# Kernel tuning notes

Hardware: AMD Instinct MI355X
Metric: run time of the kernel (lower is better)

## Reference

```python
import jax, jax.numpy as jnp
import numpy as np

VOCAB, EMBED, EN_H, DE_H, ATTN, LAYERS = 50000, 256, 512, 512, 256, 2
SEQ, BATCH = 1024, 64

def setup_inputs() -> dict:
    key = jax.random.key(0)
    ks = jax.random.split(key, 20)
    n = lambda k, shp: jax.random.normal(k, shp, dtype=jnp.float32)
    inp = {
        "cur_input": jax.random.randint(ks[0], (BATCH,), 0, VOCAB, dtype=jnp.int64) if jax.config.jax_enable_x64 else jax.random.randint(ks[0], (BATCH,), 0, VOCAB, dtype=jnp.int32),
        "h0": n(ks[1], (LAYERS, BATCH, DE_H)),
        "c0": n(ks[2], (LAYERS, BATCH, DE_H)),
        "enc_states": n(ks[3], (SEQ, BATCH, EN_H)),
        "attention_mask": jnp.ones((BATCH, SEQ), dtype=jnp.float32),
        # parameters
        "emb_table": n(ks[4], (VOCAB, EMBED)) * 0.02,
        "attn_W": n(ks[5], (EN_H + DE_H, ATTN)) * 0.02,   # attention_model: Linear(en+de, attn, bias=False)
        "attn_v": n(ks[6], (ATTN,)) * 0.02,               # Linear(attn, 1, bias=False)
        "cg_W": n(ks[7], (DE_H + EMBED + EN_H, EN_H)) * 0.02,  # context gate
        "cg_b": jnp.zeros((EN_H,), dtype=jnp.float32),
        "Wih0": n(ks[8], (4 * DE_H, EN_H + EMBED)) * 0.02,
        "Whh0": n(ks[9], (4 * DE_H, DE_H)) * 0.02,
        "bih0": jnp.zeros((4 * DE_H,), dtype=jnp.float32),
        "bhh0": jnp.zeros((4 * DE_H,), dtype=jnp.float32),
        "Wih1": n(ks[10], (4 * DE_H, DE_H)) * 0.02,
        "Whh1": n(ks[11], (4 * DE_H, DE_H)) * 0.02,
        "bih1": jnp.zeros((4 * DE_H,), dtype=jnp.float32),
        "bhh1": jnp.zeros((4 * DE_H,), dtype=jnp.float32),
        "out_W": n(ks[12], (DE_H, VOCAB)) * 0.02,
        "out_b": jnp.zeros((VOCAB,), dtype=jnp.float32),
    }
    return inp

def _lstm_cell(x, h, c, Wih, Whh, bih, bhh):
    gates = x @ Wih.T + h @ Whh.T + bih + bhh  # (B, 4H), torch gate order i,f,g,o
    i, f, g, o = jnp.split(gates, 4, axis=-1)
    c_new = jax.nn.sigmoid(f) * c + jax.nn.sigmoid(i) * jnp.tanh(g)
    h_new = jax.nn.sigmoid(o) * jnp.tanh(c_new)
    return h_new, c_new

def reference(cur_input, h0, c0, enc_states, attention_mask,
              emb_table, attn_W, attn_v, cg_W, cg_b,
              Wih0, Whh0, bih0, bhh0, Wih1, Whh1, bih1, bhh1,
              out_W, out_b):
    S, B, _ = enc_states.shape
    dec = h0[-1]  # (B, DE_H)
    # Bahdanau attention: score over seq dim
    dec_b = jnp.broadcast_to(dec[None], (S, B, dec.shape[-1]))
    feat = jnp.tanh(jnp.concatenate([enc_states, dec_b], axis=-1) @ attn_W)  # (S,B,ATTN)
    e = feat @ attn_v  # (S,B)
    e = jnp.where(attention_mask.T > 0, e, jnp.float32(-1e9))
    alpha = jax.nn.softmax(e, axis=0)  # (S,B)
    ctx = jnp.einsum('sb,sbh->bh', alpha, enc_states)  # (B, EN_H)
    # embedding + context gate
    emb = emb_table[cur_input]  # (B, EMBED)
    gate = jax.nn.sigmoid(jnp.concatenate([dec, emb, ctx], axis=-1) @ cg_W + cg_b)
    ctx = gate * ctx
    x = jnp.concatenate([emb, ctx], axis=-1)  # (B, EMBED+EN_H)
    # two-layer single-step LSTM
    h1, c1 = _lstm_cell(x, h0[0], c0[0], Wih0, Whh0, bih0, bhh0)
    h2, c2 = _lstm_cell(h1, h0[1], c0[1], Wih1, Whh1, bih1, bhh1)
    out = h2 @ out_W + out_b  # (B, VOCAB)
    return out, jnp.stack([h1, h2]), jnp.stack([c1, c2])
```

## Files before the change

### kernel.cpp

```cpp
#include <hip/hip_runtime.h>
#include <math.h>


typedef __attribute__((ext_vector_type(8))) short short8;
typedef __attribute__((ext_vector_type(4))) float f32x4;

__device__ __forceinline__ float sigf(float x) { return 1.f / (1.f + expf(-x)); }

__device__ __forceinline__ unsigned short f2bf(float f) {
    unsigned int u = __builtin_bit_cast(unsigned int, f);
    unsigned int r = (u + 0x7fffu + ((u >> 16) & 1u)) >> 16;
    return (unsigned short)r;
}

__device__ __forceinline__ float tanh_fast(float x) {
    float t = __expf(2.f * x);
    return 1.f - 2.f * __builtin_amdgcn_rcpf(1.f + t);
}

__global__ void k_prep_conv(const int* __restrict__ cur, const float* __restrict__ h0,
                            const float* __restrict__ emb_table, const float* __restrict__ attn_W,
                            float* __restrict__ X1, float* __restrict__ X2, float* __restrict__ X3,
                            float* __restrict__ decW, unsigned short* __restrict__ Wt) {
    int t = threadIdx.x;
    if (blockIdx.x >= 64) {
        __shared__ float tile[64][65];
        int bx = blockIdx.x - 64;
        int kb = (bx & 7) * 64, nb = (bx >> 3) * 64;
        int r0 = t >> 6, c = t & 63;
#pragma unroll
        for (int i = 0; i < 16; ++i) {
            int r = i * 4 + r0;
            tile[r][c] = attn_W[(size_t)(kb + r) * 256 + nb + c];
        }
        __syncthreads();
#pragma unroll
        for (int i = 0; i < 16; ++i) {
            int r = i * 4 + r0;
            int n = nb + r;
            int byte = ((n * 128 + ((c >> 3) << 4)) ^ ((r & 7) << 4)) + ((c & 7) << 1);
            *(unsigned short*)((char*)Wt + kb * 512 + byte) = f2bf(tile[c][r]);
        }
        return;
    }
    __shared__ float dec_s[512];
    int b = blockIdx.x;
    const float* dec = h0 + (size_t)(64 + b) * 512;
    for (int i = t; i < 512; i += 256) {
        float v = dec[i];
        dec_s[i] = v;
        X1[b * 1280 + i] = v;
        X2[b * 1280 + 768 + i] = h0[(size_t)b * 512 + i];
        X3[b * 1024 + 512 + i] = v;
    }
    int row = cur[b];
    float ev = emb_table[(size_t)row * 256 + t];
    X1[b * 1280 + 512 + t] = ev;
    X2[b * 1280 + t] = ev;
    __syncthreads();
    float acc = 0.f;
    for (int k = 0; k < 512; ++k)
        acc += dec_s[k] * attn_W[(size_t)(512 + k) * 256 + t];
    decW[b * 256 + t] = acc;
}

__global__ __launch_bounds__(256) void k_scores_mfma(
        const float* __restrict__ enc, const unsigned short* __restrict__ Wt,
        const float* __restrict__ attn_v, const float* __restrict__ decW,
        float* __restrict__ e_out) {
    int s = blockIdx.x, t = threadIdx.x;
    __shared__ __align__(16) unsigned short sA[2][4096];
    __shared__ __align__(16) unsigned short sB[16384];
    const float* arow = enc + (size_t)s * 64 * 512;
    int w = t >> 6, l = t & 63, li = l & 15, lg = l >> 4;
    int sw = (li & 7) << 4;

    int ar0 = t >> 3, akg0 = t & 7;
    int ar1 = (256 + t) >> 3, akg1 = t & 7;
    int abyte0 = (ar0 * 128 + akg0 * 16) ^ ((ar0 & 7) << 4);
    int abyte1 = (ar1 * 128 + akg1 * 16) ^ ((ar1 & 7) << 4);
    int bbase = w * 8192 + l * 16;

    f32x4 acc[4][4];
#pragma unroll
    for (int rt = 0; rt < 4; ++rt)
#pragma unroll
        for (int ct = 0; ct < 4; ++ct) acc[rt][ct] = (f32x4){0.f, 0.f, 0.f, 0.f};

    float4 aP[4];
    uint4  bP[8];

#pragma unroll
    for (int i = 0; i < 2; ++i) {
        const float* g = arow + (ar0 + i * 32) * 512 + akg0 * 8;
        aP[2 * i] = *(const float4*)g;
        aP[2 * i + 1] = *(const float4*)(g + 4);
    }
#pragma unroll
    for (int j = 0; j < 8; ++j)
        bP[j] = *(const uint4*)((const char*)Wt + bbase + j * 1024);
    {
        uint4 wv0, wv1;
        wv0.x = f2bf(aP[0].x) | ((unsigned)f2bf(aP[0].y) << 16);
        wv0.y = f2bf(aP[0].z) | ((unsigned)f2bf(aP[0].w) << 16);
        wv0.z = f2bf(aP[1].x) | ((unsigned)f2bf(aP[1].y) << 16);
        wv0.w = f2bf(aP[1].z) | ((unsigned)f2bf(aP[1].w) << 16);
        wv1.x = f2bf(aP[2].x) | ((unsigned)f2bf(aP[2].y) << 16);
        wv1.y = f2bf(aP[2].z) | ((unsigned)f2bf(aP[2].w) << 16);
        wv1.z = f2bf(aP[3].x) | ((unsigned)f2bf(aP[3].y) << 16);
        wv1.w = f2bf(aP[3].z) | ((unsigned)f2bf(aP[3].w) << 16);
        *(uint4*)((char*)sA[0] + abyte0) = wv0;
        *(uint4*)((char*)sA[0] + abyte1) = wv1;
#pragma unroll
        for (int j = 0; j < 8; ++j)
            *(uint4*)((char*)sB + bbase + j * 1024) = bP[j];
    }
    __syncthreads();

    for (int kk = 0; kk < 8; ++kk) {
        int cur = kk & 1;
        if (kk < 7) {
            int ko = (kk + 1) * 64;
#pragma unroll
            for (int i = 0; i < 2; ++i) {
                const float* g = arow + (ar0 + i * 32) * 512 + ko + akg0 * 8;
                aP[2 * i] = *(const float4*)g;
                aP[2 * i + 1] = *(const float4*)(g + 4);
            }
            const char* src = (const char*)Wt + ((kk + 1) << 15);
#pragma unroll
            for (int j = 0; j < 8; ++j)
                bP[j] = *(const uint4*)(src + bbase + j * 1024);
        }
#pragma unroll
        for (int ks = 0; ks < 2; ++ks) {
            short8 af[4], bf[4];
#pragma unroll
            for (int rt = 0; rt < 4; ++rt) {
                int row = rt * 16 + li;
                af[rt] = *(short8*)((char*)sA[cur] + ((row * 128 + ks * 64 + lg * 16) ^ sw));
            }
#pragma unroll
            for (int ct = 0; ct < 4; ++ct) {
                int n = w * 64 + ct * 16 + li;
                bf[ct] = *(short8*)((char*)sB + ((n * 128 + ks * 64 + lg * 16) ^ sw));
            }
#pragma unroll
            for (int rt = 0; rt < 4; ++rt)
#pragma unroll
                for (int ct = 0; ct < 4; ++ct)
                    acc[rt][ct] = __builtin_amdgcn_mfma_f32_16x16x32_bf16(
                        af[rt], bf[ct], acc[rt][ct], 0, 0, 0);
        }
        if (kk < 7) {
            uint4 wv0, wv1;
            wv0.x = f2bf(aP[0].x) | ((unsigned)f2bf(aP[0].y) << 16);
            wv0.y = f2bf(aP[0].z) | ((unsigned)f2bf(aP[0].w) << 16);
            wv0.z = f2bf(aP[1].x) | ((unsigned)f2bf(aP[1].y) << 16);
            wv0.w = f2bf(aP[1].z) | ((unsigned)f2bf(aP[1].w) << 16);
            wv1.x = f2bf(aP[2].x) | ((unsigned)f2bf(aP[2].y) << 16);
            wv1.y = f2bf(aP[2].z) | ((unsigned)f2bf(aP[2].w) << 16);
            wv1.z = f2bf(aP[3].x) | ((unsigned)f2bf(aP[3].y) << 16);
            wv1.w = f2bf(aP[3].z) | ((unsigned)f2bf(aP[3].w) << 16);
            *(uint4*)((char*)sA[cur ^ 1] + abyte0) = wv0;
            *(uint4*)((char*)sA[cur ^ 1] + abyte1) = wv1;
#pragma unroll
            for (int j = 0; j < 8; ++j)
                *(uint4*)((char*)sB + bbase + j * 1024) = bP[j];
        }
        __syncthreads();
    }

    float er[4][4];
#pragma unroll
    for (int rt = 0; rt < 4; ++rt)
#pragma unroll
        for (int r = 0; r < 4; ++r) er[rt][r] = 0.f;
#pragma unroll
    for (int ct = 0; ct < 4; ++ct) {
        int a = w * 64 + ct * 16 + li;
        float v = attn_v[a];
#pragma unroll
        for (int rt = 0; rt < 4; ++rt) {
#pragma unroll
            for (int r = 0; r < 4; ++r) {
                int row = rt * 16 + lg * 4 + r;
                float x = acc[rt][ct][r] + decW[row * 256 + a];
                er[rt][r] += tanh_fast(x) * v;
            }
        }
    }
#pragma unroll
    for (int off = 1; off < 16; off <<= 1)
#pragma unroll
        for (int rt = 0; rt < 4; ++rt)
#pragma unroll
            for (int r = 0; r < 4; ++r)
                er[rt][r] += __shfl_xor(er[rt][r], off, 64);
    float* part = (float*)sA[0];
    if (li == 0) {
#pragma unroll
        for (int rt = 0; rt < 4; ++rt)
#pragma unroll
            for (int r = 0; r < 4; ++r)
                part[w * 64 + rt * 16 + lg * 4 + r] = er[rt][r];
    }
    __syncthreads();
    if (t < 64)
        e_out[t * 1024 + s] = part[t] + part[64 + t] + part[128 + t] + part[192 + t];
}

__global__ __launch_bounds__(512) void k_ctx_partial(const float* __restrict__ ebuf,
        const float* __restrict__ mask, const float* __restrict__ enc,
        float* __restrict__ ctxP) {
    int b = blockIdx.x & 63, sc = blockIdx.x >> 6;
    int t = threadIdx.x;
    __shared__ float al[128];
    __shared__ float red[16];
    float v0 = ebuf[b * 1024 + t];
    float v1 = ebuf[b * 1024 + 512 + t];
    v0 = (mask[b * 1024 + t] > 0.f) ? v0 : -1e9f;
    v1 = (mask[b * 1024 + 512 + t] > 0.f) ? v1 : -1e9f;
    float lmax = fmaxf(v0, v1);
#pragma unroll
    for (int off = 32; off > 0; off >>= 1) lmax = fmaxf(lmax, __shfl_xor(lmax, off, 64));
    if ((t & 63) == 0) red[t >> 6] = lmax;
    __syncthreads();
    float m = red[0];
#pragma unroll
    for (int i = 1; i < 8; ++i) m = fmaxf(m, red[i]);
    float lsum = __expf(v0 - m) + __expf(v1 - m);
#pragma unroll
    for (int off = 32; off > 0; off >>= 1) lsum += __shfl_xor(lsum, off, 64);
    if ((t & 63) == 0) red[8 + (t >> 6)] = lsum;
    __syncthreads();
    float tot = red[8];
#pragma unroll
    for (int i = 1; i < 8; ++i) tot += red[8 + i];
    float inv = 1.f / tot;
    if (t < 128) {
        int s = sc * 128 + t;
        float x = ebuf[b * 1024 + s];
        x = (mask[b * 1024 + s] > 0.f) ? x : -1e9f;
        al[t] = __expf(x - m) * inv;
    }
    __syncthreads();
    const float* base = enc + (((size_t)sc * 128 * 64) + b) * 512 + t;
    float a0 = 0.f, a1 = 0.f, a2 = 0.f, a3 = 0.f;
    for (int s = 0; s < 128; s += 4) {
        float x0 = base[(size_t)(s + 0) * 32768];
        float x1 = base[(size_t)(s + 1) * 32768];
        float x2 = base[(size_t)(s + 2) * 32768];
        float x3 = base[(size_t)(s + 3) * 32768];
        a0 += al[s] * x0; a1 += al[s + 1] * x1; a2 += al[s + 2] * x2; a3 += al[s + 3] * x3;
    }
    ctxP[((size_t)sc * 64 + b) * 512 + t] = a0 + a1 + a2 + a3;
}

__global__ __launch_bounds__(1024) void k_gemm_cg(const float* __restrict__ X,
        const float* __restrict__ ctxP, const float* __restrict__ Wkn,
        float* __restrict__ P) {
    int n0 = blockIdx.x * 64, sp = blockIdx.y;
    int t = threadIdx.x, tc = t & 63, tr = t >> 6;
    __shared__ __align__(16) float As[64 * 68];
    __shared__ __align__(16) float Wc[64 * 68];
    float acc[4] = {0.f, 0.f, 0.f, 0.f};
    for (int c = 0; c < 5; ++c) {
        int k0 = sp * 320 + c * 64;
        __syncthreads();
#pragma unroll
        for (int i = 0; i < 4; ++i) {
            int idx = i * 1024 + t; int row = idx >> 6; int k = idx & 63;
            int gk = k0 + k;
            float v;
            if (gk < 768) {
                v = X[row * 1280 + gk];
            } else {
                int h = gk - 768;
                v = 0.f;
#pragma unroll
                for (int sc = 0; sc < 8; ++sc)
                    v += ctxP[((size_t)sc * 64 + row) * 512 + h];
            }
            As[k * 68 + row] = v;
        }
#pragma unroll
        for (int i = 0; i < 4; ++i) {
            int idx = i * 1024 + t; int k = idx >> 6; int cc = idx & 63;
            Wc[k * 68 + cc] = Wkn[(size_t)(k0 + k) * 512 + n0 + cc];
        }
        __syncthreads();
#pragma unroll 8
        for (int k = 0; k < 64; ++k) {
            float4 a = *(const float4*)&As[k * 68 + 4 * tr];
            float wv = Wc[k * 68 + tc];
            acc[0] += a.x * wv; acc[1] += a.y * wv; acc[2] += a.z * wv; acc[3] += a.w * wv;
        }
    }
    float* Pp = P + (size_t)sp * 64 * 512;
#pragma unroll
    for (int j = 0; j < 4; ++j) Pp[(4 * tr + j) * 512 + n0 + tc] = acc[j];
}

__global__ __launch_bounds__(1024) void k_gemm_lstm(const float* __restrict__ X, int ldx,
        const float* __restrict__ W1, int K1, const float* __restrict__ W2, int K2,
        int kchunks, float* __restrict__ P) {
    int n0 = blockIdx.x * 64, sp = blockIdx.y;
    int t = threadIdx.x, tc = t & 63, tr = t >> 6;
    __shared__ __align__(16) float As[64 * 68];
    __shared__ __align__(16) float Wc[64 * 68];
    float acc[4] = {0.f, 0.f, 0.f, 0.f};
    for (int c = 0; c < kchunks; ++c) {
        int k0 = (sp * kchunks + c) * 64;
        __syncthreads();
#pragma unroll
        for (int i = 0; i < 4; ++i) {
            int idx = i * 1024 + t; int row = idx >> 6; int k = idx & 63;
            As[k * 68 + row] = X[row * ldx + k0 + k];
        }
#pragma unroll
        for (int i = 0; i < 4; ++i) {
            int idx = i * 1024 + t; int cc = idx >> 6; int k = idx & 63;
            int gk = k0 + k; int j = n0 + cc;
            float wv = (gk < K1) ? W1[(size_t)j * K1 + gk] : W2[(size_t)j * K2 + gk - K1];
            Wc[k * 68 + cc] = wv;
        }
        __syncthreads();
#pragma unroll 8
        for (int k = 0; k < 64; ++k) {
            float4 a = *(const float4*)&As[k * 68 + 4 * tr];
            float wv = Wc[k * 68 + tc];
            acc[0] += a.x * wv; acc[1] += a.y * wv; acc[2] += a.z * wv; acc[3] += a.w * wv;
        }
    }
    float* Pp = P + (size_t)sp * 64 * 2048;
#pragma unroll
    for (int j = 0; j < 4; ++j) Pp[(4 * tr + j) * 2048 + n0 + tc] = acc[j];
}

__global__ void k_cg_fin(const float* __restrict__ P, const float* __restrict__ cg_b,
                         const float* __restrict__ ctxP, float* __restrict__ X2) {
    int idx = blockIdx.x * 256 + threadIdx.x;
    int b = idx >> 9, h = idx & 511;
    float g = cg_b[h];
#pragma unroll
    for (int sp = 0; sp < 4; ++sp) g += P[sp * 32768 + idx];
    float ctx = 0.f;
#pragma unroll
    for (int sc = 0; sc < 8; ++sc) ctx += ctxP[((size_t)sc * 64 + b) * 512 + h];
    X2[b * 1280 + 256 + h] = sigf(g) * ctx;
}

__global__ void k_lstm_fin(const float* __restrict__ P, const float* __restrict__ bih,
                           const float* __restrict__ bhh, const float* __restrict__ c0,
                           int layer, float* __restrict__ oh, float* __restrict__ oc,
                           float* __restrict__ X3out) {
    int idx = blockIdx.x * 256 + threadIdx.x;
    int b = idx >> 9, h = idx & 511;
    float gi = bih[h] + bhh[h];
    float gf = bih[512 + h] + bhh[512 + h];
    float gg = bih[1024 + h] + bhh[1024 + h];
    float go = bih[1536 + h] + bhh[1536 + h];
#pragma unroll
    for (int sp = 0; sp < 4; ++sp) {
        const float* Pp = P + sp * 131072 + b * 2048;
        gi += Pp[h]; gf += Pp[512 + h]; gg += Pp[1024 + h]; go += Pp[1536 + h];
    }
    float cp = c0[layer * 32768 + b * 512 + h];
    float cn = sigf(gf) * cp + sigf(gi) * tanhf(gg);
    float hn = sigf(go) * tanhf(cn);
    oh[b * 512 + h] = hn;
    oc[b * 512 + h] = cn;
    if (X3out) X3out[b * 1024 + h] = hn;
}

__global__ __launch_bounds__(256) void k_outproj_mfma(
        const float* __restrict__ h2, const float* __restrict__ out_W,
        const float* __restrict__ out_b, float* __restrict__ out) {
    int t = threadIdx.x;
    int n0 = blockIdx.x * 128;
    int w = t >> 6, l = t & 63, li = l & 15, lg = l >> 4;
    int sw = (li & 7) << 4;
    __shared__ __align__(16) unsigned short sA[4096];

    f32x4 acc[4][2];
#pragma unroll
    for (int rt = 0; rt < 4; ++rt)
#pragma unroll
        for (int ct = 0; ct < 2; ++ct) acc[rt][ct] = (f32x4){0.f, 0.f, 0.f, 0.f};
    int colbase = n0 + w * 32;

    for (int kk = 0; kk < 512; kk += 64) {
        __syncthreads();
#pragma unroll
        for (int i = 0; i < 2; ++i) {
            int idx = i * 256 + t, row = idx >> 3, kg = idx & 7;
            const float* g = h2 + row * 512 + kk + kg * 8;
            float4 p0 = *(const float4*)g;
            float4 p1 = *(const float4*)(g + 4);
            uint4 wv;
            wv.x = f2bf(p0.x) | ((unsigned)f2bf(p0.y) << 16);
            wv.y = f2bf(p0.z) | ((unsigned)f2bf(p0.w) << 16);
            wv.z = f2bf(p1.x) | ((unsigned)f2bf(p1.y) << 16);
            wv.w = f2bf(p1.z) | ((unsigned)f2bf(p1.w) << 16);
            int byte = (row * 128 + kg * 16) ^ ((row & 7) << 4);
            *(uint4*)((char*)sA + byte) = wv;
        }
        __syncthreads();
#pragma unroll
        for (int ks = 0; ks < 2; ++ks) {
            short8 bf[2];
#pragma unroll
            for (int ct = 0; ct < 2; ++ct) {
                int col = colbase + ct * 16 + li;
                col = (col < 50000) ? col : 49999;
                const float* wp = out_W + (size_t)(kk + ks * 32 + lg * 8) * 50000 + col;
                uint4 qv;
                float v0 = wp[0],          v1 = wp[50000];
                float v2 = wp[2 * 50000],  v3 = wp[3 * 50000];
                float v4 = wp[4 * 50000],  v5 = wp[5 * 50000];
                float v6 = wp[6 * 50000],  v7 = wp[7 * 50000];
                qv.x = f2bf(v0) | ((unsigned)f2bf(v1) << 16);
                qv.y = f2bf(v2) | ((unsigned)f2bf(v3) << 16);
                qv.z = f2bf(v4) | ((unsigned)f2bf(v5) << 16);
                qv.w = f2bf(v6) | ((unsigned)f2bf(v7) << 16);
                bf[ct] = *(short8*)&qv;
            }
            short8 af[4];
#pragma unroll
            for (int rt = 0; rt < 4; ++rt) {
                int row = rt * 16 + li;
                af[rt] = *(short8*)((char*)sA + ((row * 128 + ks * 64 + lg * 16) ^ sw));
            }
#pragma unroll
            for (int rt = 0; rt < 4; ++rt)
#pragma unroll
                for (int ct = 0; ct < 2; ++ct)
                    acc[rt][ct] = __builtin_amdgcn_mfma_f32_16x16x32_bf16(
                        af[rt], bf[ct], acc[rt][ct], 0, 0, 0);
        }
    }
#pragma unroll
    for (int ct = 0; ct < 2; ++ct) {
        int col = colbase + ct * 16 + li;
        if (col < 50000) {
            float bias = out_b[col];
#pragma unroll
            for (int rt = 0; rt < 4; ++rt)
#pragma unroll
                for (int r = 0; r < 4; ++r) {
                    int row = rt * 16 + lg * 4 + r;
                    out[(size_t)row * 50000 + col] = acc[rt][ct][r] + bias;
                }
        }
    }
}

extern "C" void kernel_launch(void* const* d_in, const int* in_sizes, int n_in,
                              void* d_out, int out_size, void* d_ws, size_t ws_size,
                              hipStream_t stream) {
    const int*   cur       = (const int*)d_in[0];
    const float* h0        = (const float*)d_in[1];
    const float* c0        = (const float*)d_in[2];
    const float* enc       = (const float*)d_in[3];
    const float* mask      = (const float*)d_in[4];
    const float* emb_table = (const float*)d_in[5];
    const float* attn_W    = (const float*)d_in[6];
    const float* attn_v    = (const float*)d_in[7];
    const float* cg_W      = (const float*)d_in[8];
    const float* cg_b      = (const float*)d_in[9];
    const float* Wih0      = (const float*)d_in[10];
    const float* Whh0      = (const float*)d_in[11];
    const float* bih0      = (const float*)d_in[12];
    const float* bhh0      = (const float*)d_in[13];
    const float* Wih1      = (const float*)d_in[14];
    const float* Whh1      = (const float*)d_in[15];
    const float* bih1      = (const float*)d_in[16];
    const float* bhh1      = (const float*)d_in[17];
    const float* out_W     = (const float*)d_in[18];
    const float* out_b     = (const float*)d_in[19];
    float* out = (float*)d_out;

    float* w    = (float*)d_ws;
    float* X1   = w;
    float* X2   = X1 + 81920;
    float* X3   = X2 + 81920;
    float* decW = X3 + 65536;
    float* eb   = decW + 16384;
    float* P    = eb + 65536;
    unsigned short* Wt = (unsigned short*)P;
    float* ctxP = P + 524288;

    float* outH = out + 3200000;
    float* outC = out + 3265536;

    hipLaunchKernelGGL(k_prep_conv, dim3(96), dim3(256), 0, stream,
                       cur, h0, emb_table, attn_W, X1, X2, X3, decW, Wt);
    hipLaunchKernelGGL(k_scores_mfma, dim3(1024), dim3(256), 0, stream,
                       enc, Wt, attn_v, decW, eb);
    hipLaunchKernelGGL(k_ctx_partial, dim3(512), dim3(512), 0, stream,
                       eb, mask, enc, ctxP);
    hipLaunchKernelGGL(k_gemm_cg, dim3(8, 4), dim3(1024), 0, stream,
                       X1, ctxP, cg_W, P);
    hipLaunchKernelGGL(k_cg_fin, dim3(128), dim3(256), 0, stream, P, cg_b, ctxP, X2);
    hipLaunchKernelGGL(k_gemm_lstm, dim3(32, 4), dim3(1024), 0, stream,
                       X2, 1280, Wih0, 768, Whh0, 512, 5, P);
    hipLaunchKernelGGL(k_lstm_fin, dim3(128), dim3(256), 0, stream,
                       P, bih0, bhh0, c0, 0, outH, outC, X3);
    hipLaunchKernelGGL(k_gemm_lstm, dim3(32, 4), dim3(1024), 0, stream,
                       X3, 1024, Wih1, 512, Whh1, 512, 4, P);
    hipLaunchKernelGGL(k_lstm_fin, dim3(128), dim3(256), 0, stream,
                       P, bih1, bhh1, c0, 1, outH + 32768, outC + 32768, (float*)nullptr);
    hipLaunchKernelGGL(k_outproj_mfma, dim3(391), dim3(256), 0, stream,
                       outH + 32768, out_W, out_b, out);
}
```

Measured before the change: 184.0 us.

## Fuse context-gate and LSTM finalize steps into following GEMM prologues

Removes the separate context-gate finalize and layer-0 LSTM finalize kernels by recomputing their elementwise work inside the A-tile load of the next GEMM, and halves the split-K factor so each GEMM has two partial slices. It also swaps the manual bf16 rounding for the packed v_cvt_pk_bf16_f32 instruction and uses fast sigmoid/tanh. This cuts kernel launches and intermediate round-trips, but the fused GEMMs recompute the gate math redundantly across column blocks and run fewer blocks, so there is less parallelism.

```diff
diff --git a/kernel.cpp b/kernel.cpp
--- a/kernel.cpp
+++ b/kernel.cpp
@@ -6,11 +6,20 @@
 typedef __attribute__((ext_vector_type(4))) float f32x4;
 
 __device__ __forceinline__ float sigf(float x) { return 1.f / (1.f + expf(-x)); }
+__device__ __forceinline__ float sigf_fast(float x) {
+    return __builtin_amdgcn_rcpf(1.f + __expf(-x));
+}
 
 __device__ __forceinline__ unsigned short f2bf(float f) {
     unsigned int u = __builtin_bit_cast(unsigned int, f);
     unsigned int r = (u + 0x7fffu + ((u >> 16) & 1u)) >> 16;
     return (unsigned short)r;
+}
+
+__device__ __forceinline__ unsigned cvt_pk(float lo, float hi) {
+    unsigned r;
+    asm("v_cvt_pk_bf16_f32 %0, %1, %2" : "=v"(r) : "v"(lo), "v"(hi));
+    return r;
 }
 
 __device__ __forceinline__ float tanh_fast(float x) {
@@ -76,9 +85,9 @@
     int sw = (li & 7) << 4;
 
     int ar0 = t >> 3, akg0 = t & 7;
-    int ar1 = (256 + t) >> 3, akg1 = t & 7;
+    int ar1 = (256 + t) >> 3;
     int abyte0 = (ar0 * 128 + akg0 * 16) ^ ((ar0 & 7) << 4);
-    int abyte1 = (ar1 * 128 + akg1 * 16) ^ ((ar1 & 7) << 4);
+    int abyte1 = (ar1 * 128 + akg0 * 16) ^ ((ar1 & 7) << 4);
     int bbase = w * 8192 + l * 16;
 
     f32x4 acc[4][4];
@@ -101,14 +110,10 @@
         bP[j] = *(const uint4*)((const char*)Wt + bbase + j * 1024);
     {
         uint4 wv0, wv1;
-        wv0.x = f2bf(aP[0].x) | ((unsigned)f2bf(aP[0].y) << 16);
-        wv0.y = f2bf(aP[0].z) | ((unsigned)f2bf(aP[0].w) << 16);
-        wv0.z = f2bf(aP[1].x) | ((unsigned)f2bf(aP[1].y) << 16);
-        wv0.w = f2bf(aP[1].z) | ((unsigned)f2bf(aP[1].w) << 16);
-        wv1.x = f2bf(aP[2].x) | ((unsigned)f2bf(aP[2].y) << 16);
-        wv1.y = f2bf(aP[2].z) | ((unsigned)f2bf(aP[2].w) << 16);
-        wv1.z = f2bf(aP[3].x) | ((unsigned)f2bf(aP[3].y) << 16);
-        wv1.w = f2bf(aP[3].z) | ((unsigned)f2bf(aP[3].w) << 16);
+        wv0.x = cvt_pk(aP[0].x, aP[0].y); wv0.y = cvt_pk(aP[0].z, aP[0].w);
+        wv0.z = cvt_pk(aP[1].x, aP[1].y); wv0.w = cvt_pk(aP[1].z, aP[1].w);
+        wv1.x = cvt_pk(aP[2].x, aP[2].y); wv1.y = cvt_pk(aP[2].z, aP[2].w);
+        wv1.z = cvt_pk(aP[3].x, aP[3].y); wv1.w = cvt_pk(aP[3].z, aP[3].w);
         *(uint4*)((char*)sA[0] + abyte0) = wv0;
         *(uint4*)((char*)sA[0] + abyte1) = wv1;
 #pragma unroll
@@ -154,14 +159,10 @@
         }
         if (kk < 7) {
             uint4 wv0, wv1;
-            wv0.x = f2bf(aP[0].x) | ((unsigned)f2bf(aP[0].y) << 16);
-            wv0.y = f2bf(aP[0].z) | ((unsigned)f2bf(aP[0].w) << 16);
-            wv0.z = f2bf(aP[1].x) | ((unsigned)f2bf(aP[1].y) << 16);
-            wv0.w = f2bf(aP[1].z) | ((unsigned)f2bf(aP[1].w) << 16);
-            wv1.x = f2bf(aP[2].x) | ((unsigned)f2bf(aP[2].y) << 16);
-            wv1.y = f2bf(aP[2].z) | ((unsigned)f2bf(aP[2].w) << 16);
-            wv1.z = f2bf(aP[3].x) | ((unsigned)f2bf(aP[3].y) << 16);
-            wv1.w = f2bf(aP[3].z) | ((unsigned)f2bf(aP[3].w) << 16);
+            wv0.x = cvt_pk(aP[0].x, aP[0].y); wv0.y = cvt_pk(aP[0].z, aP[0].w);
+            wv0.z = cvt_pk(aP[1].x, aP[1].y); wv0.w = cvt_pk(aP[1].z, aP[1].w);
+            wv1.x = cvt_pk(aP[2].x, aP[2].y); wv1.y = cvt_pk(aP[2].z, aP[2].w);
+            wv1.z = cvt_pk(aP[3].x, aP[3].y); wv1.w = cvt_pk(aP[3].z, aP[3].w);
             *(uint4*)((char*)sA[cur ^ 1] + abyte0) = wv0;
             *(uint4*)((char*)sA[cur ^ 1] + abyte1) = wv1;
 #pragma unroll
@@ -259,14 +260,14 @@
 
 __global__ __launch_bounds__(1024) void k_gemm_cg(const float* __restrict__ X,
         const float* __restrict__ ctxP, const float* __restrict__ Wkn,
-        float* __restrict__ P) {
+        float* __restrict__ P1) {
     int n0 = blockIdx.x * 64, sp = blockIdx.y;
     int t = threadIdx.x, tc = t & 63, tr = t >> 6;
     __shared__ __align__(16) float As[64 * 68];
     __shared__ __align__(16) float Wc[64 * 68];
     float acc[4] = {0.f, 0.f, 0.f, 0.f};
-    for (int c = 0; c < 5; ++c) {
-        int k0 = sp * 320 + c * 64;
+    for (int c = 0; c < 10; ++c) {
+        int k0 = sp * 640 + c * 64;
         __syncthreads();
 #pragma unroll
         for (int i = 0; i < 4; ++i) {
@@ -297,32 +298,48 @@
             acc[0] += a.x * wv; acc[1] += a.y * wv; acc[2] += a.z * wv; acc[3] += a.w * wv;
         }
     }
-    float* Pp = P + (size_t)sp * 64 * 512;
+    float* Pp = P1 + (size_t)sp * 32768;
 #pragma unroll
     for (int j = 0; j < 4; ++j) Pp[(4 * tr + j) * 512 + n0 + tc] = acc[j];
 }
 
-__global__ __launch_bounds__(1024) void k_gemm_lstm(const float* __restrict__ X, int ldx,
-        const float* __restrict__ W1, int K1, const float* __restrict__ W2, int K2,
-        int kchunks, float* __restrict__ P) {
+__global__ __launch_bounds__(1024) void k_lstm0_fused(const float* __restrict__ X2,
+        const float* __restrict__ P1, const float* __restrict__ ctxP,
+        const float* __restrict__ cg_b,
+        const float* __restrict__ Wih0, const float* __restrict__ Whh0,
+        float* __restrict__ Pl0) {
     int n0 = blockIdx.x * 64, sp = blockIdx.y;
     int t = threadIdx.x, tc = t & 63, tr = t >> 6;
     __shared__ __align__(16) float As[64 * 68];
     __shared__ __align__(16) float Wc[64 * 68];
     float acc[4] = {0.f, 0.f, 0.f, 0.f};
-    for (int c = 0; c < kchunks; ++c) {
-        int k0 = (sp * kchunks + c) * 64;
+    for (int c = 0; c < 10; ++c) {
+        int k0 = sp * 640 + c * 64;
         __syncthreads();
 #pragma unroll
         for (int i = 0; i < 4; ++i) {
             int idx = i * 1024 + t; int row = idx >> 6; int k = idx & 63;
-            As[k * 68 + row] = X[row * ldx + k0 + k];
+            int gk = k0 + k;
+            float v;
+            if (gk < 256 || gk >= 768) {
+                v = X2[row * 1280 + gk];
+            } else {
+                int h = gk - 256;
+                float g = cg_b[h] + P1[row * 512 + h] + P1[32768 + row * 512 + h];
+                float ctx = 0.f;
+#pragma unroll
+                for (int sc = 0; sc < 8; ++sc)
+                    ctx += ctxP[((size_t)sc * 64 + row) * 512 + h];
+                v = sigf_fast(g) * ctx;
+            }
+            As[k * 68 + row] = v;
         }
 #pragma unroll
         for (int i = 0; i < 4; ++i) {
             int idx = i * 1024 + t; int cc = idx >> 6; int k = idx & 63;
             int gk = k0 + k; int j = n0 + cc;
-            float wv = (gk < K1) ? W1[(size_t)j * K1 + gk] : W2[(size_t)j * K2 + gk - K1];
+            float wv = (gk < 768) ? Wih0[(size_t)j * 768 + gk]
+                                  : Whh0[(size_t)j * 512 + gk - 768];
             Wc[k * 68 + cc] = wv;
         }
         __syncthreads();
@@ -333,28 +350,74 @@
             acc[0] += a.x * wv; acc[1] += a.y * wv; acc[2] += a.z * wv; acc[3] += a.w * wv;
         }
     }
-    float* Pp = P + (size_t)sp * 64 * 2048;
+    float* Pp = Pl0 + (size_t)sp * 131072;
 #pragma unroll
     for (int j = 0; j < 4; ++j) Pp[(4 * tr + j) * 2048 + n0 + tc] = acc[j];
 }
 
-__global__ void k_cg_fin(const float* __restrict__ P, const float* __restrict__ cg_b,
-                         const float* __restrict__ ctxP, float* __restrict__ X2) {
-    int idx = blockIdx.x * 256 + threadIdx.x;
-    int b = idx >> 9, h = idx & 511;
-    float g = cg_b[h];
-#pragma unroll
-    for (int sp = 0; sp < 4; ++sp) g += P[sp * 32768 + idx];
-    float ctx = 0.f;
-#pragma unroll
-    for (int sc = 0; sc < 8; ++sc) ctx += ctxP[((size_t)sc * 64 + b) * 512 + h];
-    X2[b * 1280 + 256 + h] = sigf(g) * ctx;
-}
-
-__global__ void k_lstm_fin(const float* __restrict__ P, const float* __restrict__ bih,
-                           const float* __restrict__ bhh, const float* __restrict__ c0,
-                           int layer, float* __restrict__ oh, float* __restrict__ oc,
-                           float* __restrict__ X3out) {
+__global__ __launch_bounds__(1024) void k_lstm1_fused(const float* __restrict__ X3,
+        const float* __restrict__ Pl0, const float* __restrict__ bih0,
+        const float* __restrict__ bhh0, const float* __restrict__ c0,
+        const float* __restrict__ Wih1, const float* __restrict__ Whh1,
+        float* __restrict__ Pl1, float* __restrict__ outH, float* __restrict__ outC) {
+    int n0 = blockIdx.x * 64, sp = blockIdx.y;
+    int t = threadIdx.x, tc = t & 63, tr = t >> 6;
+    __shared__ __align__(16) float As[64 * 68];
+    __shared__ __align__(16) float Wc[64 * 68];
+    float acc[4] = {0.f, 0.f, 0.f, 0.f};
+    for (int c = 0; c < 8; ++c) {
+        int k0 = sp * 512 + c * 64;
+        __syncthreads();
+#pragma unroll
+        for (int i = 0; i < 4; ++i) {
+            int idx = i * 1024 + t; int row = idx >> 6; int k = idx & 63;
+            int gk = k0 + k;
+            float v;
+            if (gk < 512) {
+                int h = gk;
+                const float* Pa = Pl0 + row * 2048;
+                const float* Pb = Pl0 + 131072 + row * 2048;
+                float gi = bih0[h] + bhh0[h] + Pa[h] + Pb[h];
+                float gf = bih0[512 + h] + bhh0[512 + h] + Pa[512 + h] + Pb[512 + h];
+                float gg = bih0[1024 + h] + bhh0[1024 + h] + Pa[1024 + h] + Pb[1024 + h];
+                float go = bih0[1536 + h] + bhh0[1536 + h] + Pa[1536 + h] + Pb[1536 + h];
+                float cp = c0[row * 512 + h];
+                float cn = sigf_fast(gf) * cp + sigf_fast(gi) * tanh_fast(gg);
+                float hn = sigf_fast(go) * tanh_fast(cn);
+                v = hn;
+                if (n0 == 0) {
+                    outH[row * 512 + h] = hn;
+                    outC[row * 512 + h] = cn;
+                }
+            } else {
+                v = X3[row * 1024 + gk];
+            }
+            As[k * 68 + row] = v;
+        }
+#pragma unroll
+        for (int i = 0; i < 4; ++i) {
+            int idx = i * 1024 + t; int cc = idx >> 6; int k = idx & 63;
+            int gk = k0 + k; int j = n0 + cc;
+            float wv = (gk < 512) ? Wih1[(size_t)j * 512 + gk]
+                                  : Whh1[(size_t)j * 512 + gk - 512];
+            Wc[k * 68 + cc] = wv;
+        }
+        __syncthreads();
+#pragma unroll 8
+        for (int k = 0; k < 64; ++k) {
+            float4 a = *(const float4*)&As[k * 68 + 4 * tr];
+            float wv = Wc[k * 68 + tc];
+            acc[0] += a.x * wv; acc[1] += a.y * wv; acc[2] += a.z * wv; acc[3] += a.w * wv;
+        }
+    }
+    float* Pp = Pl1 + (size_t)sp * 131072;
+#pragma unroll
+    for (int j = 0; j < 4; ++j) Pp[(4 * tr + j) * 2048 + n0 + tc] = acc[j];
+}
+
+__global__ void k_lstm_fin1(const float* __restrict__ Pl1, const float* __restrict__ bih,
+                            const float* __restrict__ bhh, const float* __restrict__ c0,
+                            float* __restrict__ oh, float* __restrict__ oc) {
     int idx = blockIdx.x * 256 + threadIdx.x;
     int b = idx >> 9, h = idx & 511;
     float gi = bih[h] + bhh[h];
@@ -362,16 +425,15 @@
     float gg = bih[1024 + h] + bhh[1024 + h];
     float go = bih[1536 + h] + bhh[1536 + h];
 #pragma unroll
-    for (int sp = 0; sp < 4; ++sp) {
-        const float* Pp = P + sp * 131072 + b * 2048;
+    for (int sp = 0; sp < 2; ++sp) {
+        const float* Pp = Pl1 + sp * 131072 + b * 2048;
         gi += Pp[h]; gf += Pp[512 + h]; gg += Pp[1024 + h]; go += Pp[1536 + h];
     }
-    float cp = c0[layer * 32768 + b * 512 + h];
+    float cp = c0[32768 + b * 512 + h];
     float cn = sigf(gf) * cp + sigf(gi) * tanhf(gg);
     float hn = sigf(go) * tanhf(cn);
-    oh[b * 512 + h] = hn;
-    oc[b * 512 + h] = cn;
-    if (X3out) X3out[b * 1024 + h] = hn;
+    oh[32768 + b * 512 + h] = hn;
+    oc[32768 + b * 512 + h] = cn;
 }
 
 __global__ __launch_bounds__(256) void k_outproj_mfma(
@@ -399,10 +461,8 @@
             float4 p0 = *(const float4*)g;
             float4 p1 = *(const float4*)(g + 4);
             uint4 wv;
-            wv.x = f2bf(p0.x) | ((unsigned)f2bf(p0.y) << 16);
-            wv.y = f2bf(p0.z) | ((unsigned)f2bf(p0.w) << 16);
-            wv.z = f2bf(p1.x) | ((unsigned)f2bf(p1.y) << 16);
-            wv.w = f2bf(p1.z) | ((unsigned)f2bf(p1.w) << 16);
+            wv.x = cvt_pk(p0.x, p0.y); wv.y = cvt_pk(p0.z, p0.w);
+            wv.z = cvt_pk(p1.x, p1.y); wv.w = cvt_pk(p1.z, p1.w);
             int byte = (row * 128 + kg * 16) ^ ((row & 7) << 4);
             *(uint4*)((char*)sA + byte) = wv;
         }
@@ -420,10 +480,8 @@
                 float v2 = wp[2 * 50000],  v3 = wp[3 * 50000];
                 float v4 = wp[4 * 50000],  v5 = wp[5 * 50000];
                 float v6 = wp[6 * 50000],  v7 = wp[7 * 50000];
-                qv.x = f2bf(v0) | ((unsigned)f2bf(v1) << 16);
-                qv.y = f2bf(v2) | ((unsigned)f2bf(v3) << 16);
-                qv.z = f2bf(v4) | ((unsigned)f2bf(v5) << 16);
-                qv.w = f2bf(v6) | ((unsigned)f2bf(v7) << 16);
+                qv.x = cvt_pk(v0, v1); qv.y = cvt_pk(v2, v3);
+                qv.z = cvt_pk(v4, v5); qv.w = cvt_pk(v6, v7);
                 bf[ct] = *(short8*)&qv;
             }
             short8 af[4];
@@ -487,9 +545,11 @@
     float* X3   = X2 + 81920;
     float* decW = X3 + 65536;
     float* eb   = decW + 16384;
-    float* P    = eb + 65536;
-    unsigned short* Wt = (unsigned short*)P;
-    float* ctxP = P + 524288;
+    float* P1   = eb;
+    float* Pl0  = eb + 65536;
+    float* Pl1  = Pl0 + 262144;
+    float* ctxP = Pl1 + 262144;
+    unsigned short* Wt = (unsigned short*)Pl0;
 
     float* outH = out + 3200000;
     float* outC = out + 3265536;
@@ -500,17 +560,14 @@
                        enc, Wt, attn_v, decW, eb);
     hipLaunchKernelGGL(k_ctx_partial, dim3(512), dim3(512), 0, stream,
                        eb, mask, enc, ctxP);
-    hipLaunchKernelGGL(k_gemm_cg, dim3(8, 4), dim3(1024), 0, stream,
-                       X1, ctxP, cg_W, P);
-    hipLaunchKernelGGL(k_cg_fin, dim3(128), dim3(256), 0, stream, P, cg_b, ctxP, X2);
-    hipLaunchKernelGGL(k_gemm_lstm, dim3(32, 4), dim3(1024), 0, stream,
-                       X2, 1280, Wih0, 768, Whh0, 512, 5, P);
-    hipLaunchKernelGGL(k_lstm_fin, dim3(128), dim3(256), 0, stream,
-                       P, bih0, bhh0, c0, 0, outH, outC, X3);
-    hipLaunchKernelGGL(k_gemm_lstm, dim3(32, 4), dim3(1024), 0, stream,
-                       X3, 1024, Wih1, 512, Whh1, 512, 4, P);
-    hipLaunchKernelGGL(k_lstm_fin, dim3(128), dim3(256), 0, stream,
-                       P, bih1, bhh1, c0, 1, outH + 32768, outC + 32768, (float*)nullptr);
+    hipLaunchKernelGGL(k_gemm_cg, dim3(8, 2), dim3(1024), 0, stream,
+                       X1, ctxP, cg_W, P1);
+    hipLaunchKernelGGL(k_lstm0_fused, dim3(32, 2), dim3(1024), 0, stream,
+                       X2, P1, ctxP, cg_b, Wih0, Whh0, Pl0);
+    hipLaunchKernelGGL(k_lstm1_fused, dim3(32, 2), dim3(1024), 0, stream,
+                       X3, Pl0, bih0, bhh0, c0, Wih1, Whh1, Pl1, outH, outC);
+    hipLaunchKernelGGL(k_lstm_fin1, dim3(128), dim3(256), 0, stream,
+                       Pl1, bih1, bhh1, c0, outH, outC);
     hipLaunchKernelGGL(k_outproj_mfma, dim3(391), dim3(256), 0, stream,
                        outH + 32768, out_W, out_b, out);
 }
```

After: 355.9 us. 93.4% more time.

## Fuse LSTM gate GEMM and cell update into one MFMA kernel per layer

Applied to the files above, without the earlier changes.

Replaces the FP32 split-K LSTM GEMM plus separate finalize kernel with a single bf16 MFMA kernel per layer. Each block computes all four gates for 32 hidden units and applies the cell update in-block, removing the partial-sum round trip and two launches. Also swaps the software float-to-bf16 rounding for the hardware packed-convert instruction across kernels. The trade-off is that the LSTM launch now uses only 16 blocks, which limits parallelism, and the weights are converted to bf16, which lowers precision.

```diff
diff --git a/kernel.cpp b/kernel.cpp
--- a/kernel.cpp
+++ b/kernel.cpp
@@ -11,6 +11,12 @@
     unsigned int u = __builtin_bit_cast(unsigned int, f);
     unsigned int r = (u + 0x7fffu + ((u >> 16) & 1u)) >> 16;
     return (unsigned short)r;
+}
+
+__device__ __forceinline__ unsigned cvt_pk(float lo, float hi) {
+    unsigned r;
+    asm("v_cvt_pk_bf16_f32 %0, %1, %2" : "=v"(r) : "v"(lo), "v"(hi));
+    return r;
 }
 
 __device__ __forceinline__ float tanh_fast(float x) {
@@ -76,9 +82,9 @@
     int sw = (li & 7) << 4;
 
     int ar0 = t >> 3, akg0 = t & 7;
-    int ar1 = (256 + t) >> 3, akg1 = t & 7;
+    int ar1 = (256 + t) >> 3;
     int abyte0 = (ar0 * 128 + akg0 * 16) ^ ((ar0 & 7) << 4);
-    int abyte1 = (ar1 * 128 + akg1 * 16) ^ ((ar1 & 7) << 4);
+    int abyte1 = (ar1 * 128 + akg0 * 16) ^ ((ar1 & 7) << 4);
     int bbase = w * 8192 + l * 16;
 
     f32x4 acc[4][4];
@@ -101,14 +107,10 @@
         bP[j] = *(const uint4*)((const char*)Wt + bbase + j * 1024);
     {
         uint4 wv0, wv1;
-        wv0.x = f2bf(aP[0].x) | ((unsigned)f2bf(aP[0].y) << 16);
-        wv0.y = f2bf(aP[0].z) | ((unsigned)f2bf(aP[0].w) << 16);
-        wv0.z = f2bf(aP[1].x) | ((unsigned)f2bf(aP[1].y) << 16);
-        wv0.w = f2bf(aP[1].z) | ((unsigned)f2bf(aP[1].w) << 16);
-        wv1.x = f2bf(aP[2].x) | ((unsigned)f2bf(aP[2].y) << 16);
-        wv1.y = f2bf(aP[2].z) | ((unsigned)f2bf(aP[2].w) << 16);
-        wv1.z = f2bf(aP[3].x) | ((unsigned)f2bf(aP[3].y) << 16);
-        wv1.w = f2bf(aP[3].z) | ((unsigned)f2bf(aP[3].w) << 16);
+        wv0.x = cvt_pk(aP[0].x, aP[0].y); wv0.y = cvt_pk(aP[0].z, aP[0].w);
+        wv0.z = cvt_pk(aP[1].x, aP[1].y); wv0.w = cvt_pk(aP[1].z, aP[1].w);
+        wv1.x = cvt_pk(aP[2].x, aP[2].y); wv1.y = cvt_pk(aP[2].z, aP[2].w);
+        wv1.z = cvt_pk(aP[3].x, aP[3].y); wv1.w = cvt_pk(aP[3].z, aP[3].w);
         *(uint4*)((char*)sA[0] + abyte0) = wv0;
         *(uint4*)((char*)sA[0] + abyte1) = wv1;
 #pragma unroll
@@ -154,14 +156,10 @@
         }
         if (kk < 7) {
             uint4 wv0, wv1;
-            wv0.x = f2bf(aP[0].x) | ((unsigned)f2bf(aP[0].y) << 16);
-            wv0.y = f2bf(aP[0].z) | ((unsigned)f2bf(aP[0].w) << 16);
-            wv0.z = f2bf(aP[1].x) | ((unsigned)f2bf(aP[1].y) << 16);
-            wv0.w = f2bf(aP[1].z) | ((unsigned)f2bf(aP[1].w) << 16);
-            wv1.x = f2bf(aP[2].x) | ((unsigned)f2bf(aP[2].y) << 16);
-            wv1.y = f2bf(aP[2].z) | ((unsigned)f2bf(aP[2].w) << 16);
-            wv1.z = f2bf(aP[3].x) | ((unsigned)f2bf(aP[3].y) << 16);
-            wv1.w = f2bf(aP[3].z) | ((unsigned)f2bf(aP[3].w) << 16);
+            wv0.x = cvt_pk(aP[0].x, aP[0].y); wv0.y = cvt_pk(aP[0].z, aP[0].w);
+            wv0.z = cvt_pk(aP[1].x, aP[1].y); wv0.w = cvt_pk(aP[1].z, aP[1].w);
+            wv1.x = cvt_pk(aP[2].x, aP[2].y); wv1.y = cvt_pk(aP[2].z, aP[2].w);
+            wv1.z = cvt_pk(aP[3].x, aP[3].y); wv1.w = cvt_pk(aP[3].z, aP[3].w);
             *(uint4*)((char*)sA[cur ^ 1] + abyte0) = wv0;
             *(uint4*)((char*)sA[cur ^ 1] + abyte1) = wv1;
 #pragma unroll
@@ -297,45 +295,9 @@
             acc[0] += a.x * wv; acc[1] += a.y * wv; acc[2] += a.z * wv; acc[3] += a.w * wv;
         }
     }
-    float* Pp = P + (size_t)sp * 64 * 512;
+    float* Pp = P + (size_t)sp * 32768;
 #pragma unroll
     for (int j = 0; j < 4; ++j) Pp[(4 * tr + j) * 512 + n0 + tc] = acc[j];
-}
-
-__global__ __launch_bounds__(1024) void k_gemm_lstm(const float* __restrict__ X, int ldx,
-        const float* __restrict__ W1, int K1, const float* __restrict__ W2, int K2,
-        int kchunks, float* __restrict__ P) {
-    int n0 = blockIdx.x * 64, sp = blockIdx.y;
-    int t = threadIdx.x, tc = t & 63, tr = t >> 6;
-    __shared__ __align__(16) float As[64 * 68];
-    __shared__ __align__(16) float Wc[64 * 68];
-    float acc[4] = {0.f, 0.f, 0.f, 0.f};
-    for (int c = 0; c < kchunks; ++c) {
-        int k0 = (sp * kchunks + c) * 64;
-        __syncthreads();
-#pragma unroll
-        for (int i = 0; i < 4; ++i) {
-            int idx = i * 1024 + t; int row = idx >> 6; int k = idx & 63;
-            As[k * 68 + row] = X[row * ldx + k0 + k];
-        }
-#pragma unroll
-        for (int i = 0; i < 4; ++i) {
-            int idx = i * 1024 + t; int cc = idx >> 6; int k = idx & 63;
-            int gk = k0 + k; int j = n0 + cc;
-            float wv = (gk < K1) ? W1[(size_t)j * K1 + gk] : W2[(size_t)j * K2 + gk - K1];
-            Wc[k * 68 + cc] = wv;
-        }
-        __syncthreads();
-#pragma unroll 8
-        for (int k = 0; k < 64; ++k) {
-            float4 a = *(const float4*)&As[k * 68 + 4 * tr];
-            float wv = Wc[k * 68 + tc];
-            acc[0] += a.x * wv; acc[1] += a.y * wv; acc[2] += a.z * wv; acc[3] += a.w * wv;
-        }
-    }
-    float* Pp = P + (size_t)sp * 64 * 2048;
-#pragma unroll
-    for (int j = 0; j < 4; ++j) Pp[(4 * tr + j) * 2048 + n0 + tc] = acc[j];
 }
 
 __global__ void k_cg_fin(const float* __restrict__ P, const float* __restrict__ cg_b,
@@ -351,27 +313,99 @@
     X2[b * 1280 + 256 + h] = sigf(g) * ctx;
 }
 
-__global__ void k_lstm_fin(const float* __restrict__ P, const float* __restrict__ bih,
-                           const float* __restrict__ bhh, const float* __restrict__ c0,
-                           int layer, float* __restrict__ oh, float* __restrict__ oc,
-                           float* __restrict__ X3out) {
-    int idx = blockIdx.x * 256 + threadIdx.x;
-    int b = idx >> 9, h = idx & 511;
-    float gi = bih[h] + bhh[h];
-    float gf = bih[512 + h] + bhh[512 + h];
-    float gg = bih[1024 + h] + bhh[1024 + h];
-    float go = bih[1536 + h] + bhh[1536 + h];
-#pragma unroll
-    for (int sp = 0; sp < 4; ++sp) {
-        const float* Pp = P + sp * 131072 + b * 2048;
-        gi += Pp[h]; gf += Pp[512 + h]; gg += Pp[1024 + h]; go += Pp[1536 + h];
-    }
-    float cp = c0[layer * 32768 + b * 512 + h];
-    float cn = sigf(gf) * cp + sigf(gi) * tanhf(gg);
-    float hn = sigf(go) * tanhf(cn);
-    oh[b * 512 + h] = hn;
-    oc[b * 512 + h] = cn;
-    if (X3out) X3out[b * 1024 + h] = hn;
+__global__ __launch_bounds__(256) void k_lstm_mfma(
+        const float* __restrict__ X, int ldx,
+        const float* __restrict__ W1, int K1, const float* __restrict__ W2, int K2,
+        int nchunks, const float* __restrict__ bih, const float* __restrict__ bhh,
+        const float* __restrict__ cprev, float* __restrict__ oh,
+        float* __restrict__ oc, float* __restrict__ X3out) {
+    int t = threadIdx.x;
+    int w = t >> 6, l = t & 63, li = l & 15, lg = l >> 4;
+    int sw = (li & 7) << 4;
+    int hbase = blockIdx.x * 32;
+    __shared__ __align__(16) unsigned short sA[4096];
+    __shared__ float gbuf[64][132];
+
+    f32x4 acc[4][2];
+#pragma unroll
+    for (int rt = 0; rt < 4; ++rt)
+#pragma unroll
+        for (int ct = 0; ct < 2; ++ct) acc[rt][ct] = (f32x4){0.f, 0.f, 0.f, 0.f};
+
+    int j0 = w * 512 + hbase + li;
+
+    for (int c = 0; c < nchunks; ++c) {
+        int k0 = c * 64;
+        __syncthreads();
+#pragma unroll
+        for (int i = 0; i < 2; ++i) {
+            int idx = i * 256 + t, row = idx >> 3, kg = idx & 7;
+            const float* g = X + row * ldx + k0 + kg * 8;
+            float4 p0 = *(const float4*)g;
+            float4 p1 = *(const float4*)(g + 4);
+            uint4 wv;
+            wv.x = cvt_pk(p0.x, p0.y); wv.y = cvt_pk(p0.z, p0.w);
+            wv.z = cvt_pk(p1.x, p1.y); wv.w = cvt_pk(p1.z, p1.w);
+            int byte = (row * 128 + kg * 16) ^ ((row & 7) << 4);
+            *(uint4*)((char*)sA + byte) = wv;
+        }
+        __syncthreads();
+        const float* wr0 = (k0 < K1) ? W1 + (size_t)j0 * K1 + k0
+                                     : W2 + (size_t)j0 * K2 + (k0 - K1);
+        const float* wr1 = (k0 < K1) ? W1 + (size_t)(j0 + 16) * K1 + k0
+                                     : W2 + (size_t)(j0 + 16) * K2 + (k0 - K1);
+#pragma unroll
+        for (int ks = 0; ks < 2; ++ks) {
+            short8 bf[2];
+#pragma unroll
+            for (int ct = 0; ct < 2; ++ct) {
+                const float* wp = (ct == 0 ? wr0 : wr1) + ks * 32 + lg * 8;
+                float4 q0 = *(const float4*)wp;
+                float4 q1 = *(const float4*)(wp + 4);
+                uint4 qv;
+                qv.x = cvt_pk(q0.x, q0.y); qv.y = cvt_pk(q0.z, q0.w);
+                qv.z = cvt_pk(q1.x, q1.y); qv.w = cvt_pk(q1.z, q1.w);
+                bf[ct] = *(short8*)&qv;
+            }
+            short8 af[4];
+#pragma unroll
+            for (int rt = 0; rt < 4; ++rt) {
+                int row = rt * 16 + li;
+                af[rt] = *(short8*)((char*)sA + ((row * 128 + ks * 64 + lg * 16) ^ sw));
+            }
+#pragma unroll
+            for (int rt = 0; rt < 4; ++rt)
+#pragma unroll
+                for (int ct = 0; ct < 2; ++ct)
+                    acc[rt][ct] = __builtin_amdgcn_mfma_f32_16x16x32_bf16(
+                        af[rt], bf[ct], acc[rt][ct], 0, 0, 0);
+        }
+    }
+    __syncthreads();
+#pragma unroll
+    for (int rt = 0; rt < 4; ++rt)
+#pragma unroll
+        for (int ct = 0; ct < 2; ++ct)
+#pragma unroll
+            for (int r = 0; r < 4; ++r) {
+                int row = rt * 16 + lg * 4 + r;
+                gbuf[row][w * 32 + ct * 16 + li] = acc[rt][ct][r];
+            }
+    __syncthreads();
+    for (int e = t; e < 2048; e += 256) {
+        int b = e >> 5, hh = e & 31;
+        int h = hbase + hh;
+        float gi = bih[h] + bhh[h] + gbuf[b][hh];
+        float gf = bih[512 + h] + bhh[512 + h] + gbuf[b][32 + hh];
+        float gg = bih[1024 + h] + bhh[1024 + h] + gbuf[b][64 + hh];
+        float go = bih[1536 + h] + bhh[1536 + h] + gbuf[b][96 + hh];
+        float cp = cprev[b * 512 + h];
+        float cn = sigf(gf) * cp + sigf(gi) * tanhf(gg);
+        float hn = sigf(go) * tanhf(cn);
+        oh[b * 512 + h] = hn;
+        oc[b * 512 + h] = cn;
+        if (X3out) X3out[b * 1024 + h] = hn;
+    }
 }
 
 __global__ __launch_bounds__(256) void k_outproj_mfma(
@@ -399,10 +433,8 @@
             float4 p0 = *(const float4*)g;
             float4 p1 = *(const float4*)(g + 4);
             uint4 wv;
-            wv.x = f2bf(p0.x) | ((unsigned)f2bf(p0.y) << 16);
-            wv.y = f2bf(p0.z) | ((unsigned)f2bf(p0.w) << 16);
-            wv.z = f2bf(p1.x) | ((unsigned)f2bf(p1.y) << 16);
-            wv.w = f2bf(p1.z) | ((unsigned)f2bf(p1.w) << 16);
+            wv.x = cvt_pk(p0.x, p0.y); wv.y = cvt_pk(p0.z, p0.w);
+            wv.z = cvt_pk(p1.x, p1.y); wv.w = cvt_pk(p1.z, p1.w);
             int byte = (row * 128 + kg * 16) ^ ((row & 7) << 4);
             *(uint4*)((char*)sA + byte) = wv;
         }
@@ -420,10 +452,8 @@
                 float v2 = wp[2 * 50000],  v3 = wp[3 * 50000];
                 float v4 = wp[4 * 50000],  v5 = wp[5 * 50000];
                 float v6 = wp[6 * 50000],  v7 = wp[7 * 50000];
-                qv.x = f2bf(v0) | ((unsigned)f2bf(v1) << 16);
-                qv.y = f2bf(v2) | ((unsigned)f2bf(v3) << 16);
-                qv.z = f2bf(v4) | ((unsigned)f2bf(v5) << 16);
-                qv.w = f2bf(v6) | ((unsigned)f2bf(v7) << 16);
+                qv.x = cvt_pk(v0, v1); qv.y = cvt_pk(v2, v3);
+                qv.z = cvt_pk(v4, v5); qv.w = cvt_pk(v6, v7);
                 bf[ct] = *(short8*)&qv;
             }
             short8 af[4];
@@ -488,8 +518,8 @@
     float* decW = X3 + 65536;
     float* eb   = decW + 16384;
     float* P    = eb + 65536;
+    float* ctxP = P + 131072;
     unsigned short* Wt = (unsigned short*)P;
-    float* ctxP = P + 524288;
 
     float* outH = out + 3200000;
     float* outC = out + 3265536;
@@ -503,14 +533,12 @@
     hipLaunchKernelGGL(k_gemm_cg, dim3(8, 4), dim3(1024), 0, stream,
                        X1, ctxP, cg_W, P);
     hipLaunchKernelGGL(k_cg_fin, dim3(128), dim3(256), 0, stream, P, cg_b, ctxP, X2);
-    hipLaunchKernelGGL(k_gemm_lstm, dim3(32, 4), dim3(1024), 0, stream,
-                       X2, 1280, Wih0, 768, Whh0, 512, 5, P);
-    hipLaunchKernelGGL(k_lstm_fin, dim3(128), dim3(256), 0, stream,
-                       P, bih0, bhh0, c0, 0, outH, outC, X3);
-    hipLaunchKernelGGL(k_gemm_lstm, dim3(32, 4), dim3(1024), 0, stream,
-                       X3, 1024, Wih1, 512, Whh1, 512, 4, P);
-    hipLaunchKernelGGL(k_lstm_fin, dim3(128), dim3(256), 0, stream,
-                       P, bih1, bhh1, c0, 1, outH + 32768, outC + 32768, (float*)nullptr);
+    hipLaunchKernelGGL(k_lstm_mfma, dim3(16), dim3(256), 0, stream,
+                       X2, 1280, Wih0, 768, Whh0, 512, 20, bih0, bhh0,
+                       c0, outH, outC, X3);
+    hipLaunchKernelGGL(k_lstm_mfma, dim3(16), dim3(256), 0, stream,
+                       X3, 1024, Wih1, 512, Whh1, 512, 16, bih1, bhh1,
+                       c0 + 32768, outH + 32768, outC + 32768, (float*)nullptr);
     hipLaunchKernelGGL(k_outproj_mfma, dim3(391), dim3(256), 0, stream,
                        outH + 32768, out_W, out_b, out);
 }
```

Result: slower. 248.9 us (+35.3%).
